# Kernel tuning notes

Hardware: AMD Instinct MI355X
Metric: run time of the kernel (lower is better)

The kernel has to match this reference:

```python
import jax, jax.numpy as jnp
import numpy as np

J = 29  # joints per frame (from fc = Linear(29*3, 2))
C = 3   # feature channels (GCNConv(3, 3))


def setup_inputs() -> dict:
    key = jax.random.key(0)
    ks = jax.random.split(key, 6)
    batch_size, num_frames = 256, 1024
    n_total = batch_size * num_frames * J
    x = jax.random.normal(ks[0], (n_total, C), dtype=jnp.float32)
    edge_index = jax.random.randint(ks[1], (2, 56), 0, J, dtype=jnp.int64)
    # GCNConv(3,3) params and fc Linear(87,2) params
    W = jax.random.normal(ks[2], (C, C), dtype=jnp.float32) / np.sqrt(C)
    b = jnp.zeros((C,), dtype=jnp.float32)
    fc_W = jax.random.normal(ks[3], (J * C, 2), dtype=jnp.float32) / np.sqrt(J * C)
    fc_b = jnp.zeros((2,), dtype=jnp.float32)
    return {"x": x, "edge_index": edge_index, "batch_size": batch_size,
            "num_frames": num_frames, "W": W, "b": b, "fc_W": fc_W, "fc_b": fc_b}


def reference(x, edge_index, batch_size, num_frames, W, b, fc_W, fc_b):
    num_joints = x.shape[0] // (batch_size * num_frames)  # == J
    F = batch_size * num_frames
    self_idx = jnp.arange(num_joints, dtype=edge_index.dtype)
    src = jnp.concatenate([edge_index[0], self_idx])  # add self loops (PyG default)
    dst = jnp.concatenate([edge_index[1], self_idx])
    # symmetric degree normalization D^{-1/2}(A+I)D^{-1/2}
    deg = jnp.zeros((num_joints,), x.dtype).at[dst].add(1.0)
    dinv = jnp.where(deg > 0, jax.lax.rsqrt(deg), 0.0)
    norm = dinv[src] * dinv[dst]  # [E+J]
    # transform then aggregate, vectorized over all frames at once
    xw = (x @ W).reshape(F, num_joints, -1)  # [F, J, C]
    msgs = xw[:, src, :] * norm[None, :, None]  # [F, E+J, C]
    agg = jnp.zeros_like(xw).at[:, dst, :].add(msgs) + b  # scatter-add to targets
    h = jax.nn.relu(agg).reshape(batch_size, num_frames, num_joints * W.shape[1])
    h = jnp.mean(h, axis=1)  # [B, J*C] mean over frames
    z = jax.nn.sigmoid(h @ fc_W + fc_b)  # [B, 2]
    return (h, z)
```

## Files before the change

### kernel.cpp

```cpp
#include <hip/hip_runtime.h>
#include <math.h>

#define J   29
#define CH  3
#define JC  87
#define E0  56
#define B   256
#define T   1024
#define FRAMES (B*T)
#define FPC 64
#define CPB 4
#define NBLK (FRAMES/(FPC*CPB))
#define CHUNK_F4 1392
#define BPB (T/(FPC*CPB))
#define SLOTS 4
#define PROWS 32
#define MAXOV 96
#define WAVES 8
#define RPW 4

__global__ void prep_kernel(const int* __restrict__ ei,
                            int2* __restrict__ pairs,
                            int*  __restrict__ ov_rp,
                            int2* __restrict__ ov_pairs)
{
    __shared__ float M[J * J];
    __shared__ float dinv[J];
    __shared__ int   cnt_ov[J];
    int tid = threadIdx.x;

    for (int i = tid; i < J * J; i += 64) M[i] = 0.f;
    if (tid < J) {
        int d = 1;
        for (int e = 0; e < E0; ++e) d += (ei[E0 + e] == tid) ? 1 : 0;
        dinv[tid] = rsqrtf((float)d);
    }
    __syncthreads();

    if (tid < J) {
        for (int e = 0; e < E0; ++e) {
            if (ei[E0 + e] == tid) {
                int s = ei[e];
                M[tid * J + s] += dinv[s] * dinv[tid];
            }
        }
        M[tid * J + tid] += dinv[tid] * dinv[tid];
        int c = 0;
        for (int i = 0; i < J; ++i) c += (M[tid * J + i] != 0.f) ? 1 : 0;
        cnt_ov[tid] = (c > SLOTS) ? (c - SLOTS) : 0;
    }
    __syncthreads();

    if (tid == 0) {
        int a = 0;
        for (int j = 0; j < J; ++j) { ov_rp[j] = a; a += cnt_ov[j]; }
        for (int j = J; j <= 32; ++j) ov_rp[j] = a;
    }
    __syncthreads();

    if (tid < PROWS) {
        int2 zero; zero.x = 0; zero.y = 0;
        if (tid < J) {
            int s = 0, p = ov_rp[tid];
            for (int i = 0; i < J; ++i) {
                float v = M[tid * J + i];
                if (v != 0.f) {
                    if (s < SLOTS) {
                        int2 pr; pr.x = i * 12; pr.y = __float_as_int(v);
                        pairs[tid * SLOTS + s] = pr;
                    } else {
                        int2 pr; pr.x = (tid << 16) | (i * 12); pr.y = __float_as_int(v);
                        ov_pairs[p++] = pr;
                    }
                    ++s;
                }
            }
            for (; s < SLOTS; ++s) pairs[tid * SLOTS + s] = zero;
        } else {
            for (int s = 0; s < SLOTS; ++s) pairs[tid * SLOTS + s] = zero;
        }
    }
    __syncthreads();
    if (tid == 0) {
        int a = ov_rp[J];
        for (int i = a; i < MAXOV; ++i) { int2 pr; pr.x = 0; pr.y = 0; ov_pairs[i] = pr; }
    }
}

__global__ __launch_bounds__(512, 2)
void gcn_main(const float* __restrict__ x,
              const float* __restrict__ Wp,
              const float* __restrict__ bp,
              const int2* __restrict__ pairs,
              const int*  __restrict__ ov_rp,
              const int2* __restrict__ ov_pairs,
              float* __restrict__ partials) {
    __shared__ float4 xs4[CHUNK_F4];
    __shared__ int2   s_ov[MAXOV];

    int tid  = threadIdx.x;
    int lane = tid & 63;
    int wv   = tid >> 6;
    int rowbase = __builtin_amdgcn_readfirstlane(wv * RPW);

    float sW[9], sb[CH];
#pragma unroll
    for (int i = 0; i < 9; ++i) sW[i] = Wp[i];
#pragma unroll
    for (int i = 0; i < CH; ++i) sb[i] = bp[i];
    int ov0 = ov_rp[rowbase], ov1 = ov_rp[rowbase + RPW];
    if (tid < MAXOV) s_ov[tid] = ov_pairs[tid];

    const float4* src4 = (const float4*)x + (size_t)blockIdx.x * (CPB * CHUNK_F4);

    int i2 = 1024 + tid; if (i2 > CHUNK_F4 - 1) i2 = CHUNK_F4 - 1;

    float4 pf0 = src4[tid];
    float4 pf1 = src4[512 + tid];
    float4 pf2 = src4[i2];

    float acc[RPW][CH];
#pragma unroll
    for (int r = 0; r < RPW; ++r)
#pragma unroll
        for (int c = 0; c < CH; ++c) acc[r][c] = 0.f;

#pragma unroll
    for (int c = 0; c < CPB; ++c) {
        __syncthreads();
        xs4[tid]       = pf0;
        xs4[512 + tid] = pf1;
        xs4[i2]        = pf2;
        __syncthreads();

        if (c + 1 < CPB) {
            const float4* s2 = src4 + (c + 1) * CHUNK_F4;
            pf0 = s2[tid];
            pf1 = s2[512 + tid];
            pf2 = s2[i2];
        }

        const char* xf = (const char*)xs4 + lane * 348;

        float y[RPW][CH];
#pragma unroll
        for (int R = 0; R < RPW; ++R) {
            float a0 = 0.f, a1 = 0.f, a2 = 0.f;
#pragma unroll
            for (int sl = 0; sl < SLOTS; ++sl) {
                int2 pr = pairs[(rowbase + R) * SLOTS + sl];
                float v = __int_as_float(pr.y);
                const float* q = (const float*)(xf + pr.x);
                a0 += v * q[0];
                a1 += v * q[1];
                a2 += v * q[2];
            }
            y[R][0] = a0; y[R][1] = a1; y[R][2] = a2;
        }
        for (int e = ov0; e < ov1; ++e) {
            int2 pr = s_ov[e];
            int row = pr.x >> 16;
            int off = pr.x & 0xFFFF;
            float v = __int_as_float(pr.y);
            const float* q = (const float*)(xf + off);
            float d0 = v * q[0], d1 = v * q[1], d2 = v * q[2];
#pragma unroll
            for (int R = 0; R < RPW; ++R)
                if (row == rowbase + R) { y[R][0] += d0; y[R][1] += d1; y[R][2] += d2; }
        }
#pragma unroll
        for (int R = 0; R < RPW; ++R)
#pragma unroll
            for (int ch = 0; ch < CH; ++ch) {
                float t = y[R][0] * sW[0 * CH + ch]
                        + y[R][1] * sW[1 * CH + ch]
                        + y[R][2] * sW[2 * CH + ch]
                        + sb[ch];
                acc[R][ch] += fmaxf(t, 0.f);
            }
    }

    __syncthreads();
    float* red = (float*)xs4;
#pragma unroll
    for (int R = 0; R < RPW; ++R) {
        int j = rowbase + R;
        if (j < J) {
#pragma unroll
            for (int ch = 0; ch < CH; ++ch)
                red[lane * JC + j * CH + ch] = acc[R][ch];
        }
    }
    __syncthreads();
    if (tid < JC) {
        float a = 0.f;
#pragma unroll
        for (int L = 0; L < FPC; ++L) a += red[L * JC + tid];
        partials[(size_t)blockIdx.x * JC + tid] = a;
    }
}

__global__ void finalize_kernel(const float* __restrict__ partials,
                                const float* __restrict__ fcW,
                                const float* __restrict__ fcb,
                                float* __restrict__ out) {
    __shared__ float h[JC];
    int b = blockIdx.x, tid = threadIdx.x;
    if (tid < JC) {
        float a = 0.f;
#pragma unroll
        for (int p = 0; p < BPB; ++p)
            a += partials[(size_t)(b * BPB + p) * JC + tid];
        a *= (1.0f / (float)T);
        h[tid] = a;
        out[(size_t)b * JC + tid] = a;
    }
    __syncthreads();
    if (tid < 2) {
        float a = fcb[tid];
        for (int r = 0; r < JC; ++r) a += h[r] * fcW[r * 2 + tid];
        out[(size_t)B * JC + b * 2 + tid] = 1.0f / (1.0f + expf(-a));
    }
}

extern "C" void kernel_launch(void* const* d_in, const int* in_sizes, int n_in,
                              void* d_out, int out_size, void* d_ws, size_t ws_size,
                              hipStream_t stream) {
    const float* x   = (const float*)d_in[0];
    const int*   ei  = (const int*)d_in[1];
    const float* W   = (const float*)d_in[4];
    const float* bb  = (const float*)d_in[5];
    const float* fcW = (const float*)d_in[6];
    const float* fcb = (const float*)d_in[7];

    char* ws = (char*)d_ws;
    int2* pairs    = (int2*)ws;
    int2* ov_pairs = pairs + PROWS * SLOTS;
    int*  ov_rp    = (int*)(ov_pairs + MAXOV);
    float* partials = (float*)(ws + 4096);

    prep_kernel<<<1, 64, 0, stream>>>(ei, pairs, ov_rp, ov_pairs);
    gcn_main<<<NBLK, WAVES * 64, 0, stream>>>(x, W, bb, pairs, ov_rp, ov_pairs, partials);
    finalize_kernel<<<B, 128, 0, stream>>>(partials, fcW, fcb, (float*)d_out);
}
```

Baseline: 40.63 us.

## Fold adjacency prep into main kernel and double-buffer prefetch over more chunks

Removes the separate single-block prep kernel: each wave builds its own rows' normalized adjacency slots in registers from edge_index with ballot/shuffle, and keeps overflow pairs in per-wave shared memory. Chunks per block grow from 4 to 8 (halving the block count), and two chunks of global prefetch are now in flight in registers. The launch bound asks for 4 blocks per CU. This cuts one kernel launch and the dependent global loads of pair tables. The cost is redundant per-block setup work and higher register pressure from the extra prefetch buffers.

```diff
diff --git a/kernel.cpp b/kernel.cpp
--- a/kernel.cpp
+++ b/kernel.cpp
@@ -9,115 +9,85 @@
 #define T   1024
 #define FRAMES (B*T)
 #define FPC 64
-#define CPB 4
+#define CPB 8
 #define NBLK (FRAMES/(FPC*CPB))
 #define CHUNK_F4 1392
 #define BPB (T/(FPC*CPB))
 #define SLOTS 4
-#define PROWS 32
-#define MAXOV 96
 #define WAVES 8
 #define RPW 4
-
-__global__ void prep_kernel(const int* __restrict__ ei,
-                            int2* __restrict__ pairs,
-                            int*  __restrict__ ov_rp,
-                            int2* __restrict__ ov_pairs)
-{
-    __shared__ float M[J * J];
-    __shared__ float dinv[J];
-    __shared__ int   cnt_ov[J];
-    int tid = threadIdx.x;
-
-    for (int i = tid; i < J * J; i += 64) M[i] = 0.f;
-    if (tid < J) {
-        int d = 1;
-        for (int e = 0; e < E0; ++e) d += (ei[E0 + e] == tid) ? 1 : 0;
-        dinv[tid] = rsqrtf((float)d);
-    }
-    __syncthreads();
-
-    if (tid < J) {
-        for (int e = 0; e < E0; ++e) {
-            if (ei[E0 + e] == tid) {
-                int s = ei[e];
-                M[tid * J + s] += dinv[s] * dinv[tid];
-            }
-        }
-        M[tid * J + tid] += dinv[tid] * dinv[tid];
-        int c = 0;
-        for (int i = 0; i < J; ++i) c += (M[tid * J + i] != 0.f) ? 1 : 0;
-        cnt_ov[tid] = (c > SLOTS) ? (c - SLOTS) : 0;
-    }
-    __syncthreads();
-
-    if (tid == 0) {
-        int a = 0;
-        for (int j = 0; j < J; ++j) { ov_rp[j] = a; a += cnt_ov[j]; }
-        for (int j = J; j <= 32; ++j) ov_rp[j] = a;
-    }
-    __syncthreads();
-
-    if (tid < PROWS) {
-        int2 zero; zero.x = 0; zero.y = 0;
-        if (tid < J) {
-            int s = 0, p = ov_rp[tid];
-            for (int i = 0; i < J; ++i) {
-                float v = M[tid * J + i];
-                if (v != 0.f) {
-                    if (s < SLOTS) {
-                        int2 pr; pr.x = i * 12; pr.y = __float_as_int(v);
-                        pairs[tid * SLOTS + s] = pr;
-                    } else {
-                        int2 pr; pr.x = (tid << 16) | (i * 12); pr.y = __float_as_int(v);
-                        ov_pairs[p++] = pr;
-                    }
-                    ++s;
-                }
-            }
-            for (; s < SLOTS; ++s) pairs[tid * SLOTS + s] = zero;
-        } else {
-            for (int s = 0; s < SLOTS; ++s) pairs[tid * SLOTS + s] = zero;
-        }
-    }
-    __syncthreads();
-    if (tid == 0) {
-        int a = ov_rp[J];
-        for (int i = a; i < MAXOV; ++i) { int2 pr; pr.x = 0; pr.y = 0; ov_pairs[i] = pr; }
-    }
-}
-
-__global__ __launch_bounds__(512, 2)
+#define OVCAP 64
+
+__global__ __launch_bounds__(512, 4)
 void gcn_main(const float* __restrict__ x,
+              const int*   __restrict__ ei,
               const float* __restrict__ Wp,
               const float* __restrict__ bp,
-              const int2* __restrict__ pairs,
-              const int*  __restrict__ ov_rp,
-              const int2* __restrict__ ov_pairs,
               float* __restrict__ partials) {
     __shared__ float4 xs4[CHUNK_F4];
-    __shared__ int2   s_ov[MAXOV];
+    __shared__ int2   s_ov[WAVES * OVCAP];
 
     int tid  = threadIdx.x;
     int lane = tid & 63;
     int wv   = tid >> 6;
     int rowbase = __builtin_amdgcn_readfirstlane(wv * RPW);
 
+    const float4* src4 = (const float4*)x + (size_t)blockIdx.x * (CPB * CHUNK_F4);
+    int i2 = 1024 + tid; if (i2 > CHUNK_F4 - 1) i2 = CHUNK_F4 - 1;
+
+    float4 pfA0 = src4[tid], pfA1 = src4[512 + tid], pfA2 = src4[i2];
+    const float4* s1 = src4 + CHUNK_F4;
+    float4 pfB0 = s1[tid],  pfB1 = s1[512 + tid],  pfB2 = s1[i2];
+
+    float dinv = 0.f;
+    if (lane < J) {
+        int d = 1;
+        for (int e = 0; e < E0; ++e) d += (ei[E0 + e] == lane) ? 1 : 0;
+        dinv = rsqrtf((float)d);
+    }
+    int   prx[RPW][SLOTS];
+    float prv[RPW][SLOTS];
+    int ovn = 0;
+#pragma unroll
+    for (int R = 0; R < RPW; ++R) {
+        int j = rowbase + R;
+        float mv = 0.f;
+        if (lane < J && j < J) {
+            int cnt = 0;
+            for (int e = 0; e < E0; ++e)
+                cnt += (ei[e] == lane && ei[E0 + e] == j) ? 1 : 0;
+            float dj = __shfl(dinv, j);
+            mv = (float)cnt * dinv * dj;
+            if (lane == j) mv += dinv * dinv;
+        }
+        unsigned long long mask = __ballot(mv != 0.f);
+#pragma unroll
+        for (int sl = 0; sl < SLOTS; ++sl) {
+            int pos = 0; float v = 0.f;
+            if (mask) {
+                pos = __ffsll(mask) - 1;
+                v = __shfl(mv, pos);
+                mask &= mask - 1;
+            }
+            prx[R][sl] = pos * 12;
+            prv[R][sl] = v;
+        }
+        while (mask) {
+            int pos = __ffsll(mask) - 1;
+            mask &= mask - 1;
+            float v = __shfl(mv, pos);
+            if (lane == 0) {
+                int2 pr; pr.x = (j << 16) | (pos * 12); pr.y = __float_as_int(v);
+                s_ov[wv * OVCAP + ovn] = pr;
+            }
+            ++ovn;
+        }
+    }
     float sW[9], sb[CH];
 #pragma unroll
     for (int i = 0; i < 9; ++i) sW[i] = Wp[i];
 #pragma unroll
     for (int i = 0; i < CH; ++i) sb[i] = bp[i];
-    int ov0 = ov_rp[rowbase], ov1 = ov_rp[rowbase + RPW];
-    if (tid < MAXOV) s_ov[tid] = ov_pairs[tid];
-
-    const float4* src4 = (const float4*)x + (size_t)blockIdx.x * (CPB * CHUNK_F4);
-
-    int i2 = 1024 + tid; if (i2 > CHUNK_F4 - 1) i2 = CHUNK_F4 - 1;
-
-    float4 pf0 = src4[tid];
-    float4 pf1 = src4[512 + tid];
-    float4 pf2 = src4[i2];
 
     float acc[RPW][CH];
 #pragma unroll
@@ -125,59 +95,62 @@
 #pragma unroll
         for (int c = 0; c < CH; ++c) acc[r][c] = 0.f;
 
-#pragma unroll
-    for (int c = 0; c < CPB; ++c) {
-        __syncthreads();
-        xs4[tid]       = pf0;
-        xs4[512 + tid] = pf1;
-        xs4[i2]        = pf2;
-        __syncthreads();
-
-        if (c + 1 < CPB) {
-            const float4* s2 = src4 + (c + 1) * CHUNK_F4;
-            pf0 = s2[tid];
-            pf1 = s2[512 + tid];
-            pf2 = s2[i2];
-        }
-
-        const char* xf = (const char*)xs4 + lane * 348;
-
-        float y[RPW][CH];
-#pragma unroll
-        for (int R = 0; R < RPW; ++R) {
-            float a0 = 0.f, a1 = 0.f, a2 = 0.f;
-#pragma unroll
-            for (int sl = 0; sl < SLOTS; ++sl) {
-                int2 pr = pairs[(rowbase + R) * SLOTS + sl];
-                float v = __int_as_float(pr.y);
-                const float* q = (const float*)(xf + pr.x);
-                a0 += v * q[0];
-                a1 += v * q[1];
-                a2 += v * q[2];
-            }
-            y[R][0] = a0; y[R][1] = a1; y[R][2] = a2;
-        }
-        for (int e = ov0; e < ov1; ++e) {
-            int2 pr = s_ov[e];
-            int row = pr.x >> 16;
-            int off = pr.x & 0xFFFF;
-            float v = __int_as_float(pr.y);
-            const float* q = (const float*)(xf + off);
-            float d0 = v * q[0], d1 = v * q[1], d2 = v * q[2];
-#pragma unroll
-            for (int R = 0; R < RPW; ++R)
-                if (row == rowbase + R) { y[R][0] += d0; y[R][1] += d1; y[R][2] += d2; }
-        }
-#pragma unroll
-        for (int R = 0; R < RPW; ++R)
-#pragma unroll
-            for (int ch = 0; ch < CH; ++ch) {
-                float t = y[R][0] * sW[0 * CH + ch]
-                        + y[R][1] * sW[1 * CH + ch]
-                        + y[R][2] * sW[2 * CH + ch]
-                        + sb[ch];
-                acc[R][ch] += fmaxf(t, 0.f);
-            }
+#define COMPUTE_CHUNK                                                         \
+    {                                                                         \
+        const char* xf = (const char*)xs4 + lane * 348;                       \
+        float y[RPW][CH];                                                     \
+        _Pragma("unroll")                                                     \
+        for (int R = 0; R < RPW; ++R) {                                       \
+            float a0 = 0.f, a1 = 0.f, a2 = 0.f;                               \
+            _Pragma("unroll")                                                 \
+            for (int sl = 0; sl < SLOTS; ++sl) {                              \
+                float v = prv[R][sl];                                         \
+                const float* q = (const float*)(xf + prx[R][sl]);             \
+                a0 += v * q[0]; a1 += v * q[1]; a2 += v * q[2];               \
+            }                                                                 \
+            y[R][0] = a0; y[R][1] = a1; y[R][2] = a2;                         \
+        }                                                                     \
+        for (int e = 0; e < ovn; ++e) {                                       \
+            int2 pr = s_ov[wv * OVCAP + e];                                   \
+            int row = pr.x >> 16; int off = pr.x & 0xFFFF;                    \
+            float v = __int_as_float(pr.y);                                   \
+            const float* q = (const float*)(xf + off);                        \
+            float d0 = v * q[0], d1 = v * q[1], d2 = v * q[2];                \
+            _Pragma("unroll")                                                 \
+            for (int R = 0; R < RPW; ++R)                                     \
+                if (row == rowbase + R) { y[R][0] += d0; y[R][1] += d1; y[R][2] += d2; } \
+        }                                                                     \
+        _Pragma("unroll")                                                     \
+        for (int R = 0; R < RPW; ++R)                                         \
+            _Pragma("unroll")                                                 \
+            for (int ch = 0; ch < CH; ++ch) {                                 \
+                float t = y[R][0] * sW[0 * CH + ch]                           \
+                        + y[R][1] * sW[1 * CH + ch]                           \
+                        + y[R][2] * sW[2 * CH + ch]                           \
+                        + sb[ch];                                             \
+                acc[R][ch] += fmaxf(t, 0.f);                                  \
+            }                                                                 \
+    }
+
+#pragma unroll
+    for (int c = 0; c < CPB; c += 2) {
+        __syncthreads();
+        xs4[tid] = pfA0; xs4[512 + tid] = pfA1; xs4[i2] = pfA2;
+        __syncthreads();
+        if (c + 2 < CPB) {
+            const float4* sn = src4 + (c + 2) * CHUNK_F4;
+            pfA0 = sn[tid]; pfA1 = sn[512 + tid]; pfA2 = sn[i2];
+        }
+        COMPUTE_CHUNK;
+
+        __syncthreads();
+        xs4[tid] = pfB0; xs4[512 + tid] = pfB1; xs4[i2] = pfB2;
+        __syncthreads();
+        if (c + 3 < CPB) {
+            const float4* sn = src4 + (c + 3) * CHUNK_F4;
+            pfB0 = sn[tid]; pfB1 = sn[512 + tid]; pfB2 = sn[i2];
+        }
+        COMPUTE_CHUNK;
     }
 
     __syncthreads();
@@ -233,13 +206,8 @@
     const float* fcW = (const float*)d_in[6];
     const float* fcb = (const float*)d_in[7];
 
-    char* ws = (char*)d_ws;
-    int2* pairs    = (int2*)ws;
-    int2* ov_pairs = pairs + PROWS * SLOTS;
-    int*  ov_rp    = (int*)(ov_pairs + MAXOV);
-    float* partials = (float*)(ws + 4096);
-
-    prep_kernel<<<1, 64, 0, stream>>>(ei, pairs, ov_rp, ov_pairs);
-    gcn_main<<<NBLK, WAVES * 64, 0, stream>>>(x, W, bb, pairs, ov_rp, ov_pairs, partials);
+    float* partials = (float*)d_ws;
+
+    gcn_main<<<NBLK, WAVES * 64, 0, stream>>>(x, ei, W, bb, partials);
     finalize_kernel<<<B, 128, 0, stream>>>(partials, fcW, fcb, (float*)d_out);
 }
```

After: 65.37 us. 1.61x slower.
